# Performance work log

Measured on AMD Instinct MI355X. Metric: run time of the kernel, lower is better.

## Reference

```python
import jax, jax.numpy as jnp
import numpy as np

B, DK, N, DV = 16, 64, 8192, 64


def setup_inputs() -> dict:
    key = jax.random.key(0)
    kq, kk, kv = jax.random.split(key, 3)
    q = jax.random.normal(kq, (B, DK, N), dtype=jnp.float32)   # channel-first q
    k = jax.random.normal(kk, (B, N, DK), dtype=jnp.float32)
    v = jax.random.normal(kv, (B, N, DV), dtype=jnp.float32)
    return {"q": q, "k": k, "v": v}


def reference(q, k, v):
    # torch: bmm(q.permute(0,2,1), bmm(k.permute(0,2,1), v))
    # k^T v: [B, DK, DV] -- small on-chip-able intermediate
    ktv = jnp.einsum('bnk,bnv->bkv', k, v)
    # q^T (k^T v): [B, N, DV]
    out = jnp.einsum('bkn,bkv->bnv', q, ktv)
    return out
```

## Files before the change

### kernel.cpp

```cpp
#include <hip/hip_runtime.h>


#define B_      16
#define N_      8192
#define DK_     64
#define DV_     64
#define CHUNKS_ 32
#define ROWS_   256
#define SUB_    4

__global__ __launch_bounds__(256) void p1_partial(
    const float* __restrict__ K, const float* __restrict__ V,
    float* __restrict__ part)
{
    __shared__ float sm[4][4096];

    const int c = blockIdx.x, b = blockIdx.y, t = threadIdx.x;
    const int w = t >> 6, lane = t & 63;
    const int kk = (lane >> 3) * 8;
    const int vv = (lane & 7) * 8;

    const float4* K4 = (const float4*)(K + ((size_t)b * N_ + (size_t)c * ROWS_) * DK_);
    const float4* V4 = (const float4*)(V + ((size_t)b * N_ + (size_t)c * ROWS_) * DV_);

    #pragma unroll
    for (int j = 0; j < 4; ++j) {
        ((float4*)sm[0])[t + 256 * j] = K4[t + 256 * j];
        ((float4*)sm[1])[t + 256 * j] = V4[t + 256 * j];
    }
    __syncthreads();

    float acc[8][8] = {};

    for (int s = 0; s < SUB_; ++s) {
        float4 nk[4], nv[4];
        if (s + 1 < SUB_) {
            const float4* Kn = K4 + (size_t)(s + 1) * 1024;
            const float4* Vn = V4 + (size_t)(s + 1) * 1024;
            #pragma unroll
            for (int j = 0; j < 4; ++j) {
                nk[j] = Kn[t + 256 * j];
                nv[j] = Vn[t + 256 * j];
            }
        }

        const float* cK = sm[(s & 1) * 2];
        const float* cV = sm[(s & 1) * 2 + 1];
        #pragma unroll
        for (int rr = 0; rr < 16; ++rr) {
            const int r = w * 16 + rr;
            alignas(16) float fk[8], fv[8];
            *(float4*)&fk[0] = *(const float4*)&cK[r * 64 + kk];
            *(float4*)&fk[4] = *(const float4*)&cK[r * 64 + kk + 4];
            *(float4*)&fv[0] = *(const float4*)&cV[r * 64 + vv];
            *(float4*)&fv[4] = *(const float4*)&cV[r * 64 + vv + 4];
            #pragma unroll
            for (int i = 0; i < 8; ++i)
                #pragma unroll
                for (int j = 0; j < 8; ++j)
                    acc[i][j] += fk[i] * fv[j];
        }

        if (s + 1 < SUB_) {
            float* wK = sm[((s + 1) & 1) * 2];
            float* wV = sm[((s + 1) & 1) * 2 + 1];
            #pragma unroll
            for (int j = 0; j < 4; ++j) {
                ((float4*)wK)[t + 256 * j] = nk[j];
                ((float4*)wV)[t + 256 * j] = nv[j];
            }
        }
        __syncthreads();
    }

    float* reg = sm[w];
    #pragma unroll
    for (int i = 0; i < 8; ++i) {
        *(float4*)&reg[(kk + i) * 64 + vv]     = make_float4(acc[i][0], acc[i][1], acc[i][2], acc[i][3]);
        *(float4*)&reg[(kk + i) * 64 + vv + 4] = make_float4(acc[i][4], acc[i][5], acc[i][6], acc[i][7]);
    }
    __syncthreads();

    float4* P = (float4*)(part + ((size_t)c * B_ + b) * 4096);
    #pragma unroll
    for (int j = 0; j < 4; ++j) {
        const int idx = t + 256 * j;
        const float4 s0 = ((const float4*)sm[0])[idx];
        const float4 s1 = ((const float4*)sm[1])[idx];
        const float4 s2 = ((const float4*)sm[2])[idx];
        const float4 s3 = ((const float4*)sm[3])[idx];
        P[idx] = make_float4(s0.x + s1.x + s2.x + s3.x,
                             s0.y + s1.y + s2.y + s3.y,
                             s0.z + s1.z + s2.z + s3.z,
                             s0.w + s1.w + s2.w + s3.w);
    }
}

__global__ __launch_bounds__(256) void p1_reduce(
    const float* __restrict__ part, float* __restrict__ ktv)
{
    const int i = blockIdx.x * 256 + threadIdx.x;
    float4 s = make_float4(0.f, 0.f, 0.f, 0.f);
    #pragma unroll
    for (int c = 0; c < CHUNKS_; ++c) {
        const float4 p = ((const float4*)part)[(size_t)c * 16384 + i];
        s.x += p.x; s.y += p.y; s.z += p.z; s.w += p.w;
    }
    ((float4*)ktv)[i] = s;
}

__global__ __launch_bounds__(256) void p2(
    const float* __restrict__ q, const float* __restrict__ ktv,
    float* __restrict__ out)
{
    __shared__ float qs[64 * 256];
    __shared__ float ks[64 * 64];

    const int nb = blockIdx.x, b = blockIdx.y, t = threadIdx.x;
    const int n0 = nb * 256;
    const int nl = (t >> 3) * 8;
    const int vl = (t & 7) * 8;

    const float4* kt4 = (const float4*)(ktv + (size_t)b * 4096);
    #pragma unroll
    for (int j = 0; j < 4; ++j)
        ((float4*)ks)[t + 256 * j] = kt4[t + 256 * j];

    const float* qb = q + (size_t)b * DK_ * N_ + n0;
    #pragma unroll
    for (int j = 0; j < 16; ++j) {
        const int i  = t + 256 * j;
        const int k  = i >> 6;
        const int c4 = i & 63;
        ((float4*)&qs[k * 256])[c4] = ((const float4*)&qb[(size_t)k * N_])[c4];
    }
    __syncthreads();

    float acc[8][8] = {};
    #pragma unroll 4
    for (int k = 0; k < 64; ++k) {
        alignas(16) float qn[8], kv[8];
        *(float4*)&qn[0] = *(const float4*)&qs[k * 256 + nl];
        *(float4*)&qn[4] = *(const float4*)&qs[k * 256 + nl + 4];
        *(float4*)&kv[0] = *(const float4*)&ks[k * 64 + vl];
        *(float4*)&kv[4] = *(const float4*)&ks[k * 64 + vl + 4];
        #pragma unroll
        for (int i = 0; i < 8; ++i)
            #pragma unroll
            for (int j = 0; j < 8; ++j)
                acc[i][j] += qn[i] * kv[j];
    }

    float* ob = out + ((size_t)b * N_ + n0 + nl) * DV_ + vl;
    #pragma unroll
    for (int i = 0; i < 8; ++i) {
        *(float4*)&ob[(size_t)i * DV_]     = make_float4(acc[i][0], acc[i][1], acc[i][2], acc[i][3]);
        *(float4*)&ob[(size_t)i * DV_ + 4] = make_float4(acc[i][4], acc[i][5], acc[i][6], acc[i][7]);
    }
}

extern "C" void kernel_launch(void* const* d_in, const int* in_sizes, int n_in,
                              void* d_out, int out_size, void* d_ws, size_t ws_size,
                              hipStream_t stream)
{
    (void)in_sizes; (void)n_in; (void)out_size; (void)ws_size;
    const float* q = (const float*)d_in[0];
    const float* k = (const float*)d_in[1];
    const float* v = (const float*)d_in[2];
    float* out = (float*)d_out;

    float* part = (float*)d_ws;
    float* ktv  = part + (size_t)CHUNKS_ * B_ * 4096;

    p1_partial<<<dim3(CHUNKS_, B_), 256, 0, stream>>>(k, v, part);
    p1_reduce<<<dim3(64), 256, 0, stream>>>(part, ktv);
    p2<<<dim3(32, B_), 256, 0, stream>>>(q, ktv, out);
}
```

Measured before the change: 175.0 us.

## Give each wave private LDS tiles in both GEMM kernels, drop block barriers

In p1_partial, each wavefront now loads and processes its own 64-row slice of K and V in private shared memory, in two passes. This replaces the block-wide double-buffered prefetch pipeline and its per-stage __syncthreads. In p2, each wave stages its own 64-column slab of q and computes it independently, with a deeper unroll of the k loop. p1_reduce switches from float4 to scalar accumulation spread over four times as many blocks. The aim is to cut block-level barrier stalls and raise parallelism in the reduce step, at the cost of losing the prefetch overlap in p1 and using shorter contiguous q reads in p2.

```diff
diff --git a/kernel.cpp b/kernel.cpp
--- a/kernel.cpp
+++ b/kernel.cpp
@@ -1,13 +1,11 @@
 #include <hip/hip_runtime.h>
 
 
-#define B_      16
-#define N_      8192
-#define DK_     64
-#define DV_     64
-#define CHUNKS_ 32
-#define ROWS_   256
-#define SUB_    4
+#define B_   16
+#define N_   8192
+#define DK_  64
+#define DV_  64
+#define CH_  32
 
 __global__ __launch_bounds__(256) void p1_partial(
     const float* __restrict__ K, const float* __restrict__ V,
@@ -20,57 +18,34 @@
     const int kk = (lane >> 3) * 8;
     const int vv = (lane & 7) * 8;
 
-    const float4* K4 = (const float4*)(K + ((size_t)b * N_ + (size_t)c * ROWS_) * DK_);
-    const float4* V4 = (const float4*)(V + ((size_t)b * N_ + (size_t)c * ROWS_) * DV_);
+    float* Ks = &sm[w][0];
+    float* Vs = &sm[w][2048];
 
-    #pragma unroll
-    for (int j = 0; j < 4; ++j) {
-        ((float4*)sm[0])[t + 256 * j] = K4[t + 256 * j];
-        ((float4*)sm[1])[t + 256 * j] = V4[t + 256 * j];
-    }
-    __syncthreads();
+    const size_t row0 = (size_t)b * N_ + (size_t)c * 256 + (size_t)w * 64;
+    const float4* K4 = (const float4*)(K + row0 * DK_);
+    const float4* V4 = (const float4*)(V + row0 * DV_);
 
     float acc[8][8] = {};
 
-    for (int s = 0; s < SUB_; ++s) {
-        float4 nk[4], nv[4];
-        if (s + 1 < SUB_) {
-            const float4* Kn = K4 + (size_t)(s + 1) * 1024;
-            const float4* Vn = V4 + (size_t)(s + 1) * 1024;
-            #pragma unroll
-            for (int j = 0; j < 4; ++j) {
-                nk[j] = Kn[t + 256 * j];
-                nv[j] = Vn[t + 256 * j];
-            }
+    for (int r = 0; r < 2; ++r) {
+        #pragma unroll
+        for (int j = 0; j < 8; ++j) {
+            ((float4*)Ks)[lane + 64 * j] = K4[r * 512 + lane + 64 * j];
+            ((float4*)Vs)[lane + 64 * j] = V4[r * 512 + lane + 64 * j];
         }
-
-        const float* cK = sm[(s & 1) * 2];
-        const float* cV = sm[(s & 1) * 2 + 1];
-        #pragma unroll
-        for (int rr = 0; rr < 16; ++rr) {
-            const int r = w * 16 + rr;
+        #pragma unroll 4
+        for (int n = 0; n < 32; ++n) {
             alignas(16) float fk[8], fv[8];
-            *(float4*)&fk[0] = *(const float4*)&cK[r * 64 + kk];
-            *(float4*)&fk[4] = *(const float4*)&cK[r * 64 + kk + 4];
-            *(float4*)&fv[0] = *(const float4*)&cV[r * 64 + vv];
-            *(float4*)&fv[4] = *(const float4*)&cV[r * 64 + vv + 4];
+            *(float4*)&fk[0] = *(const float4*)&Ks[n * 64 + kk];
+            *(float4*)&fk[4] = *(const float4*)&Ks[n * 64 + kk + 4];
+            *(float4*)&fv[0] = *(const float4*)&Vs[n * 64 + vv];
+            *(float4*)&fv[4] = *(const float4*)&Vs[n * 64 + vv + 4];
             #pragma unroll
             for (int i = 0; i < 8; ++i)
                 #pragma unroll
                 for (int j = 0; j < 8; ++j)
                     acc[i][j] += fk[i] * fv[j];
         }
-
-        if (s + 1 < SUB_) {
-            float* wK = sm[((s + 1) & 1) * 2];
-            float* wV = sm[((s + 1) & 1) * 2 + 1];
-            #pragma unroll
-            for (int j = 0; j < 4; ++j) {
-                ((float4*)wK)[t + 256 * j] = nk[j];
-                ((float4*)wV)[t + 256 * j] = nv[j];
-            }
-        }
-        __syncthreads();
     }
 
     float* reg = sm[w];
@@ -99,27 +74,26 @@
 __global__ __launch_bounds__(256) void p1_reduce(
     const float* __restrict__ part, float* __restrict__ ktv)
 {
-    const int i = blockIdx.x * 256 + threadIdx.x;
-    float4 s = make_float4(0.f, 0.f, 0.f, 0.f);
+    const int idx = blockIdx.x * 256 + threadIdx.x;
+    float s = 0.f;
     #pragma unroll
-    for (int c = 0; c < CHUNKS_; ++c) {
-        const float4 p = ((const float4*)part)[(size_t)c * 16384 + i];
-        s.x += p.x; s.y += p.y; s.z += p.z; s.w += p.w;
-    }
-    ((float4*)ktv)[i] = s;
+    for (int c = 0; c < CH_; ++c)
+        s += part[(size_t)c * 65536 + idx];
+    ktv[idx] = s;
 }
 
 __global__ __launch_bounds__(256) void p2(
     const float* __restrict__ q, const float* __restrict__ ktv,
     float* __restrict__ out)
 {
-    __shared__ float qs[64 * 256];
-    __shared__ float ks[64 * 64];
+    __shared__ float ks[4096];
+    __shared__ float qs[4][4096];
 
     const int nb = blockIdx.x, b = blockIdx.y, t = threadIdx.x;
-    const int n0 = nb * 256;
-    const int nl = (t >> 3) * 8;
-    const int vl = (t & 7) * 8;
+    const int w = t >> 6, lane = t & 63;
+    const int nl = (lane >> 3) * 8;
+    const int vl = (lane & 7) * 8;
+    const int n0 = nb * 256 + w * 64;
 
     const float4* kt4 = (const float4*)(ktv + (size_t)b * 4096);
     #pragma unroll
@@ -129,26 +103,25 @@
     const float* qb = q + (size_t)b * DK_ * N_ + n0;
     #pragma unroll
     for (int j = 0; j < 16; ++j) {
-        const int i  = t + 256 * j;
-        const int k  = i >> 6;
-        const int c4 = i & 63;
-        ((float4*)&qs[k * 256])[c4] = ((const float4*)&qb[(size_t)k * N_])[c4];
+        const int idx = lane + 64 * j;
+        ((float4*)qs[w])[idx] =
+            ((const float4*)(qb + (size_t)(idx >> 4) * N_))[idx & 15];
     }
     __syncthreads();
 
     float acc[8][8] = {};
-    #pragma unroll 4
+    #pragma unroll 8
     for (int k = 0; k < 64; ++k) {
-        alignas(16) float qn[8], kv[8];
-        *(float4*)&qn[0] = *(const float4*)&qs[k * 256 + nl];
-        *(float4*)&qn[4] = *(const float4*)&qs[k * 256 + nl + 4];
-        *(float4*)&kv[0] = *(const float4*)&ks[k * 64 + vl];
-        *(float4*)&kv[4] = *(const float4*)&ks[k * 64 + vl + 4];
+        alignas(16) float fq[8], fv[8];
+        *(float4*)&fq[0] = *(const float4*)&qs[w][k * 64 + nl];
+        *(float4*)&fq[4] = *(const float4*)&qs[w][k * 64 + nl + 4];
+        *(float4*)&fv[0] = *(const float4*)&ks[k * 64 + vl];
+        *(float4*)&fv[4] = *(const float4*)&ks[k * 64 + vl + 4];
         #pragma unroll
         for (int i = 0; i < 8; ++i)
             #pragma unroll
             for (int j = 0; j < 8; ++j)
-                acc[i][j] += qn[i] * kv[j];
+                acc[i][j] += fq[i] * fv[j];
     }
 
     float* ob = out + ((size_t)b * N_ + n0 + nl) * DV_ + vl;
@@ -170,9 +143,9 @@
     float* out = (float*)d_out;
 
     float* part = (float*)d_ws;
-    float* ktv  = part + (size_t)CHUNKS_ * B_ * 4096;
+    float* ktv  = part + (size_t)CH_ * B_ * 4096;
 
-    p1_partial<<<dim3(CHUNKS_, B_), 256, 0, stream>>>(k, v, part);
-    p1_reduce<<<dim3(64), 256, 0, stream>>>(part, ktv);
+    p1_partial<<<dim3(CH_, B_), 256, 0, stream>>>(k, v, part);
+    p1_reduce<<<dim3(256), 256, 0, stream>>>(part, ktv);
     p2<<<dim3(32, B_), 256, 0, stream>>>(q, ktv, out);
 }
```

New measurement: 151.7 us. 13.3% less time.
